# Kernel optimization log

Measured on AMD Instinct MI355X. Metric: run time of the kernel, lower is better.

The kernel has to match this reference:

```python
import jax, jax.numpy as jnp
import numpy as np

INPUT = 27
HIDDEN = 1


def setup_inputs() -> dict:
    key = jax.random.key(0)
    k_x, k_wih, k_whh, k_bih, k_bhh = jax.random.split(key, 5)
    s = 1.0 / np.sqrt(HIDDEN)  # PyTorch LSTM init range
    x = jax.random.normal(k_x, (2048, 512, INPUT), dtype=jnp.float32)
    W_ih = jax.random.uniform(k_wih, (4 * HIDDEN, INPUT), minval=-s, maxval=s, dtype=jnp.float32)
    W_hh = jax.random.uniform(k_whh, (4 * HIDDEN, HIDDEN), minval=-s, maxval=s, dtype=jnp.float32)
    b_ih = jax.random.uniform(k_bih, (4 * HIDDEN,), minval=-s, maxval=s, dtype=jnp.float32)
    b_hh = jax.random.uniform(k_bhh, (4 * HIDDEN,), minval=-s, maxval=s, dtype=jnp.float32)
    return {"x": x, "W_ih": W_ih, "W_hh": W_hh, "b_ih": b_ih, "b_hh": b_hh}


def reference(x, W_ih, W_hh, b_ih, b_hh):
    # x: (T, B, 27). Single-layer LSTM, hidden_size=1, PyTorch gate order i,f,g,o.
    T, B, _ = x.shape
    H = HIDDEN
    # Precompute the input projection for all timesteps: (T, B, 4H)
    x_proj = jnp.einsum('tbi,gi->tbg', x, W_ih) + b_ih + b_hh

    def step(carry, xp_t):
        h, c = carry  # (B, H) each
        gates = xp_t + h @ W_hh.T  # (B, 4H)
        i = jax.nn.sigmoid(gates[:, 0 * H:1 * H])
        f = jax.nn.sigmoid(gates[:, 1 * H:2 * H])
        g = jnp.tanh(gates[:, 2 * H:3 * H])
        o = jax.nn.sigmoid(gates[:, 3 * H:4 * H])
        c_new = f * c + i * g
        h_new = o * jnp.tanh(c_new)
        return (h_new, c_new), h_new

    h0 = jnp.zeros((B, H), dtype=x.dtype)
    c0 = jnp.zeros((B, H), dtype=x.dtype)
    _, hs = jax.lax.scan(step, (h0, c0), x_proj)
    return hs  # (T, B, H)
```

## Files before the change

### kernel.cpp

```cpp
#include <hip/hip_runtime.h>

#define T_LEN 2048
#define B_SZ  512
#define NIN   27

__device__ __forceinline__ float fast_exp2(float x) { return __builtin_amdgcn_exp2f(x); }
__device__ __forceinline__ float fast_rcp(float x)  { return __builtin_amdgcn_rcpf(x); }

#define L2E 1.4426950408889634f
#define KN  (-2.0f * L2E)

template<int K>
__device__ __forceinline__ float qbcast(float v) {
    constexpr int ctrl = K | (K << 2) | (K << 4) | (K << 6);
    return __int_as_float(
        __builtin_amdgcn_update_dpp(0, __float_as_int(v), ctrl, 0xf, 0xf, true));
}

__global__ __launch_bounds__(256) void lstm_proj(const float* __restrict__ x,
                                                 const float* __restrict__ Wih,
                                                 const float* __restrict__ bih,
                                                 const float* __restrict__ bhh,
                                                 float4* __restrict__ A) {
    __shared__ float  xs[256 * NIN];
    __shared__ float4 wT[NIN];
    const int tid  = threadIdx.x;
    const size_t pos0 = (size_t)blockIdx.x * 256;

    const float4* src4 = (const float4*)(x + pos0 * NIN);
    float4* lds4 = (float4*)xs;
#pragma unroll
    for (int i = 0; i < 6; ++i) lds4[tid + i * 256] = src4[tid + i * 256];
    {
        int idx = tid + 6 * 256;
        if (idx < (256 * NIN) / 4) lds4[idx] = src4[idx];
    }

    if (tid < NIN) {
        wT[tid] = make_float4(Wih[0 * NIN + tid], Wih[1 * NIN + tid],
                              Wih[2 * NIN + tid], Wih[3 * NIN + tid]);
    }

    float acc0 = bih[0] + bhh[0];
    float acc1 = bih[1] + bhh[1];
    float acc2 = bih[2] + bhh[2];
    float acc3 = bih[3] + bhh[3];

    __syncthreads();

    const float* xr = xs + tid * NIN;
#pragma unroll 3
    for (int k = 0; k < NIN; ++k) {
        float  xv = xr[k];
        float4 w  = wT[k];
        acc0 = fmaf(xv, w.x, acc0);
        acc1 = fmaf(xv, w.y, acc1);
        acc2 = fmaf(xv, w.z, acc2);
        acc3 = fmaf(xv, w.w, acc3);
    }

    float4 o;
    o.x = -L2E * acc0;
    o.y = -L2E * acc1;
    o.z = -2.f * L2E * acc2;
    o.w = -L2E * acc3;
    A[pos0 + tid] = o;
}

#define CH 16
#define NCHUNK (T_LEN / CH)

#define SCAN_STEP(vnext, tt)                                                  \
    {                                                                         \
        float e   = fast_exp2(pre);                                           \
        float r   = fast_rcp(e + 1.0f);                                       \
        float rv  = fmaf(r, S1, S0);                                          \
        float m_g  = qbcast<2>(rv);                                           \
        float m_i  = qbcast<0>(rv);                                           \
        float m_f  = qbcast<1>(rv);                                           \
        float m_o2 = qbcast<3>(rv);                                           \
        C = fmaf(m_f, C, m_i * m_g);                                          \
        float e2 = fast_exp2(C);                                              \
        float r2 = fast_rcp(e2 + 1.0f);                                       \
        float wm = W * m_o2;                          \
        float a2 = fmaf(wm, -0.5f, (vnext));                                  \
        float h  = m_o2 * (r2 - 0.5f);                                        \
        if (g == 0) out[(tt) * B_SZ + b] = h;                                 \
        pre = fmaf(wm, r2, a2);                                               \
    }

__global__ __launch_bounds__(64, 1) void lstm_scan(const float* __restrict__ Af,
                                                   const float* __restrict__ Whh,
                                                   float* __restrict__ out) {
    const int lane = threadIdx.x;
    const int g    = lane & 3;
    const int b    = (blockIdx.x << 4) + (lane >> 2);

    const float* src = Af + (size_t)(blockIdx.x << 6) + lane;

    const float sg = (g == 2) ? (-2.f * L2E) : (-L2E);
    const float W  = sg * Whh[g];
    const float S1 = (g == 0) ? KN : ((g == 1) ? 1.f : 2.f);
    const float S0 = (g == 2) ? -1.f : 0.f;

    float C = 0.f;

    float pa[CH], pb[CH];

#pragma unroll
    for (int j = 0; j < CH; ++j) pa[j] = src[(size_t)j * 2048];
    float pre = pa[0];

    for (int n = 0; n < NCHUNK; n += 2) {
        const int t0 = n * CH;

#pragma unroll
        for (int j = 0; j < CH; ++j) pb[j] = src[(size_t)(t0 + CH + j) * 2048];
        __builtin_amdgcn_sched_barrier(0);

#pragma unroll
        for (int j = 0; j < CH - 1; ++j) SCAN_STEP(pa[j + 1], t0 + j);
        SCAN_STEP(pb[0], t0 + CH - 1);

        if (n + 2 < NCHUNK) {
#pragma unroll
            for (int j = 0; j < CH; ++j) pa[j] = src[(size_t)(t0 + 2 * CH + j) * 2048];
        }
        __builtin_amdgcn_sched_barrier(0);

#pragma unroll
        for (int j = 0; j < CH - 1; ++j) SCAN_STEP(pb[j + 1], t0 + CH + j);
        SCAN_STEP(pa[0], t0 + 2 * CH - 1);
    }
}

extern "C" void kernel_launch(void* const* d_in, const int* in_sizes, int n_in,
                              void* d_out, int out_size, void* d_ws, size_t ws_size,
                              hipStream_t stream) {
    const float* x   = (const float*)d_in[0];
    const float* Wih = (const float*)d_in[1];
    const float* Whh = (const float*)d_in[2];
    const float* bih = (const float*)d_in[3];
    const float* bhh = (const float*)d_in[4];
    float* out = (float*)d_out;
    float4* A  = (float4*)d_ws;

    const int npos = T_LEN * B_SZ;
    lstm_proj<<<npos / 256, 256, 0, stream>>>(x, Wih, bih, bhh, A);
    lstm_scan<<<B_SZ / 16, 64, 0, stream>>>((const float*)A, Whh, out);
}
```

Measured before the change: 338.6 us.

## Stream scan inputs via async global-to-LDS double-buffered loads

Replaces direct register prefetch of the projected gate inputs with asynchronous global_load_lds transfers into a double-buffered LDS tile of 32 timesteps. Registers are refilled from LDS in bursts of 8 between step groups, with explicit vmcnt waits. The aim is to hide global load latency from the serial recurrence and reduce register pressure. It relies on hand-tuned waitcnt values, which global stores to the output may perturb.

```diff
diff --git a/kernel.cpp b/kernel.cpp
--- a/kernel.cpp
+++ b/kernel.cpp
@@ -9,6 +9,11 @@
 
 #define L2E 1.4426950408889634f
 #define KN  (-2.0f * L2E)
+
+#define GLDS(gptr, lptr)                                                          \
+    __builtin_amdgcn_global_load_lds(                                             \
+        (const __attribute__((address_space(1))) unsigned int*)(gptr),            \
+        (__attribute__((address_space(3))) unsigned int*)(lptr), 16, 0, 0)
 
 template<int K>
 __device__ __forceinline__ float qbcast(float v) {
@@ -67,8 +72,8 @@
     A[pos0 + tid] = o;
 }
 
-#define CH 16
-#define NCHUNK (T_LEN / CH)
+#define CHK  32
+#define NCK  (T_LEN / CHK)
 
 #define SCAN_STEP(vnext, tt)                                                  \
     {                                                                         \
@@ -89,14 +94,38 @@
         pre = fmaf(wm, r2, a2);                                               \
     }
 
+#define BURST(reg, bufidx, base)                                              \
+    {                                                                         \
+        _Pragma("unroll")                                                     \
+        for (int j = 0; j < 8; ++j) reg[j] = lds[bufidx][(base) + j][lane];   \
+        __builtin_amdgcn_sched_barrier(0);                                    \
+    }
+
+#define STEPS(cur, nxt, tbase)                                                \
+    {                                                                         \
+        _Pragma("unroll")                                                     \
+        for (int j = 0; j < 7; ++j) SCAN_STEP(cur[j + 1], (tbase) + j);       \
+        SCAN_STEP(nxt[0], (tbase) + 7);                                       \
+    }
+
+#define ISSUE(c, bufidx)                                                      \
+    {                                                                         \
+        _Pragma("unroll")                                                     \
+        for (int j = 0; j < 8; ++j)                                           \
+            GLDS(wb + ((size_t)((c) * CHK + j * 4)) * 2048 + goff,            \
+                 &lds[bufidx][j * 4][0]);                                     \
+    }
+
 __global__ __launch_bounds__(64, 1) void lstm_scan(const float* __restrict__ Af,
                                                    const float* __restrict__ Whh,
                                                    float* __restrict__ out) {
+    __shared__ float lds[2][CHK][64];
     const int lane = threadIdx.x;
     const int g    = lane & 3;
     const int b    = (blockIdx.x << 4) + (lane >> 2);
 
-    const float* src = Af + (size_t)(blockIdx.x << 6) + lane;
+    const float* wb = Af + (blockIdx.x << 6);
+    const size_t goff = (size_t)(lane >> 4) * 2048 + (size_t)(lane & 15) * 4;
 
     const float sg = (g == 2) ? (-2.f * L2E) : (-L2E);
     const float W  = sg * Whh[g];
@@ -104,33 +133,34 @@
     const float S0 = (g == 2) ? -1.f : 0.f;
 
     float C = 0.f;
+    float ra[8], rb[8];
 
-    float pa[CH], pb[CH];
+    ISSUE(0, 0);
+    ISSUE(1, 1);
+    asm volatile("s_waitcnt vmcnt(8)" ::: "memory");
+    __builtin_amdgcn_sched_barrier(0);
+    BURST(ra, 0, 0);
+    float pre = ra[0];
 
-#pragma unroll
-    for (int j = 0; j < CH; ++j) pa[j] = src[(size_t)j * 2048];
-    float pre = pa[0];
+    for (int c = 0; c < NCK; ++c) {
+        const int buf = c & 1;
+        const int t0  = c * CHK;
 
-    for (int n = 0; n < NCHUNK; n += 2) {
-        const int t0 = n * CH;
+        BURST(rb, buf, 8);
+        STEPS(ra, rb, t0);
 
-#pragma unroll
-        for (int j = 0; j < CH; ++j) pb[j] = src[(size_t)(t0 + CH + j) * 2048];
+        BURST(ra, buf, 16);
+        STEPS(rb, ra, t0 + 8);
+
+        BURST(rb, buf, 24);
+        STEPS(ra, rb, t0 + 16);
+
+        asm volatile("s_waitcnt vmcnt(24)" ::: "memory");
         __builtin_amdgcn_sched_barrier(0);
+        BURST(ra, buf ^ 1, 0);
+        STEPS(rb, ra, t0 + 24);
 
-#pragma unroll
-        for (int j = 0; j < CH - 1; ++j) SCAN_STEP(pa[j + 1], t0 + j);
-        SCAN_STEP(pb[0], t0 + CH - 1);
-
-        if (n + 2 < NCHUNK) {
-#pragma unroll
-            for (int j = 0; j < CH; ++j) pa[j] = src[(size_t)(t0 + 2 * CH + j) * 2048];
-        }
-        __builtin_amdgcn_sched_barrier(0);
-
-#pragma unroll
-        for (int j = 0; j < CH - 1; ++j) SCAN_STEP(pb[j + 1], t0 + CH + j);
-        SCAN_STEP(pa[0], t0 + 2 * CH - 1);
+        if (c + 2 < NCK) ISSUE(c + 2, buf);
     }
 }
 
```

After: 311.7 us. 1.09x faster.
